# Performance work log

Hardware: AMD Instinct MI355X
Metric: run time of the kernel (lower is better)

## Reference

```python
import jax, jax.numpy as jnp
import numpy as np

N_NODES = 100000
N_EDGES = 1600000
NUM_FEATURES = 100
HIDDEN = 32
OUT = 2
DROP_P = 0.2


def setup_inputs() -> dict:
    key = jax.random.key(0)
    ks = jax.random.split(key, 6)
    x = jax.random.normal(ks[0], (N_NODES, NUM_FEATURES), dtype=jnp.float32)
    edge_index = jax.random.randint(ks[1], (2, N_EDGES), 0, N_NODES, dtype=jnp.int64)
    # Glorot-ish init for weights
    W1 = jax.random.normal(ks[2], (NUM_FEATURES, HIDDEN), dtype=jnp.float32) / jnp.sqrt(NUM_FEATURES)
    b1 = jnp.zeros((HIDDEN,), dtype=jnp.float32)
    W2 = jax.random.normal(ks[3], (HIDDEN, OUT), dtype=jnp.float32) / jnp.sqrt(HIDDEN)
    b2 = jnp.zeros((OUT,), dtype=jnp.float32)
    return {"x": x, "edge_index": edge_index, "W1": W1, "b1": b1, "W2": W2, "b2": b2}


def _gcn_norm(edge_index, num_nodes):
    # add self loops (fixed-size concat -> jit friendly)
    loops = jnp.arange(num_nodes, dtype=edge_index.dtype)
    src = jnp.concatenate([edge_index[0], loops])
    dst = jnp.concatenate([edge_index[1], loops])
    deg = jax.ops.segment_sum(jnp.ones_like(dst, dtype=jnp.float32), dst, num_segments=num_nodes)
    dinv = jnp.where(deg > 0, jax.lax.rsqrt(deg), 0.0)
    norm = dinv[src] * dinv[dst]  # [E+N]
    return src, dst, norm


def _gcn_conv(x, W, b, src, dst, norm, num_nodes):
    h = x @ W  # [N, d_out]
    msg = h[src] * norm[:, None]  # gather + scale
    out = jax.ops.segment_sum(msg, dst, num_segments=num_nodes)  # scatter-add
    return out + b


def reference(x, edge_index, W1, b1, W2, b2):
    n = x.shape[0]
    src, dst, norm = _gcn_norm(edge_index, n)
    h = jax.nn.relu(_gcn_conv(x, W1, b1, src, dst, norm, n))
    # deterministic dropout (p=0.2) with fixed key, inverted scaling as in F.dropout
    keep = jax.random.bernoulli(jax.random.key(42), 1.0 - DROP_P, h.shape)
    h = jnp.where(keep, h / (1.0 - DROP_P), 0.0)
    logits = _gcn_conv(h, W2, b2, src, dst, norm, n)
    return jax.nn.log_softmax(logits, axis=1)
```

## Files before the change

### kernel.cpp

```cpp
#include <hip/hip_runtime.h>
#include <stdint.h>
#include <math.h>

#define N_NODES   100000
#define N_EDGES   1600000
#define NFEAT     100
#define HIDDEN    32
#define OUTC      2

#define BUCK_BITS 7
#define BUCK_SZ   128
#define NBUCK     782
#define PADB      4096

#define PART_NB   256
#define PART_CHUNK ((N_EDGES + PART_NB - 1) / PART_NB)

typedef float fx4 __attribute__((ext_vector_type(4)));

__device__ __forceinline__ uint32_t rotl32(uint32_t x, int r) {
    return (x << r) | (x >> (32 - r));
}

__device__ __forceinline__ uint32_t threefry_bits(uint32_t f) {
    const uint32_t ks0 = 0u;
    const uint32_t ks1 = 42u;
    const uint32_t ks2 = 0x1BD11BDAu ^ 0u ^ 42u;
    uint32_t x0 = 0u + ks0;
    uint32_t x1 = f  + ks1;
#define TF_ROUND(r) { x0 += x1; x1 = rotl32(x1, (r)); x1 ^= x0; }
    TF_ROUND(13) TF_ROUND(15) TF_ROUND(26) TF_ROUND(6)
    x0 += ks1; x1 += ks2 + 1u;
    TF_ROUND(17) TF_ROUND(29) TF_ROUND(16) TF_ROUND(24)
    x0 += ks2; x1 += ks0 + 2u;
    TF_ROUND(13) TF_ROUND(15) TF_ROUND(26) TF_ROUND(6)
    x0 += ks0; x1 += ks1 + 3u;
    TF_ROUND(17) TF_ROUND(29) TF_ROUND(16) TF_ROUND(24)
    x0 += ks1; x1 += ks2 + 4u;
    TF_ROUND(13) TF_ROUND(15) TF_ROUND(26) TF_ROUND(6)
    x0 += ks2; x1 += ks0 + 5u;
#undef TF_ROUND
    return x0 ^ x1;
}

__device__ __forceinline__ bool dropout_keep(uint32_t f) {
    uint32_t bits = threefry_bits(f);
    float u = __uint_as_float((bits >> 9) | 0x3f800000u) - 1.0f;
    return u < 0.8f;
}

__device__ __forceinline__ uint16_t f2bf(float f) {
    uint32_t b = __float_as_uint(f);
    uint32_t lsb = (b >> 16) & 1u;
    b += 0x7fffu + lsb;
    return (uint16_t)(b >> 16);
}
__device__ __forceinline__ float bflo(uint32_t u) {
    return __uint_as_float(u << 16);
}
__device__ __forceinline__ float bfhi(uint32_t u) {
    return __uint_as_float(u & 0xffff0000u);
}

__global__ __launch_bounds__(256) void k_init(int* __restrict__ bcur) {
    int i = blockIdx.x * 256 + threadIdx.x;
    if (i < NBUCK) bcur[i] = i * PADB;
}

__global__ __launch_bounds__(1024) void k_part(const int* __restrict__ src,
                                               const int* __restrict__ dst,
                                               int* __restrict__ bcur,
                                               uint32_t* __restrict__ part) {
    __shared__ int h4[4][NBUCK];
    __shared__ int c4[4][NBUCK];
    const int t = threadIdx.x;
    const int w = (t >> 6) & 3;
    const int base = blockIdx.x * PART_CHUNK;
    const int lim = min(base + PART_CHUNK, N_EDGES);
    for (int i = t; i < 4 * NBUCK; i += 1024) ((int*)h4)[i] = 0;
    __syncthreads();
    for (int e = base + t; e < lim; e += 1024)
        atomicAdd(&h4[w][dst[e] >> BUCK_BITS], 1);
    __syncthreads();
    if (t < NBUCK) {
        int c0 = h4[0][t], c1 = h4[1][t], c2 = h4[2][t], c3 = h4[3][t];
        int tot = c0 + c1 + c2 + c3;
        int g = tot ? atomicAdd(&bcur[t], tot) : 0;
        c4[0][t] = g;
        c4[1][t] = g + c0;
        c4[2][t] = g + c0 + c1;
        c4[3][t] = g + c0 + c1 + c2;
    }
    __syncthreads();
    for (int e = base + t; e < lim; e += 1024) {
        int d = dst[e];
        int b = d >> BUCK_BITS;
        int pos = atomicAdd(&c4[w][b], 1);
        part[pos] = ((uint32_t)(d & (BUCK_SZ - 1)) << 17) | (uint32_t)src[e];
    }
}

__global__ __launch_bounds__(256) void k_sort(const uint32_t* __restrict__ part,
                                              const int* __restrict__ bcur,
                                              int* __restrict__ csr_src,
                                              int* __restrict__ rowbeg,
                                              int* __restrict__ deg,
                                              float* __restrict__ dinv) {
    __shared__ int cnt4[4][BUCK_SZ];
    __shared__ int pref[BUCK_SZ];
    __shared__ int cur4[4][BUCK_SZ];
    const int b = blockIdx.x;
    const int t = threadIdx.x;
    const int w = t >> 6;
    const int nbase = b * BUCK_SZ;
    const int bb = b * PADB;
    const int be = bcur[b];
    for (int i = t; i < 4 * BUCK_SZ; i += 256) ((int*)cnt4)[i] = 0;
    __syncthreads();
    for (int j = bb + t; j < be; j += 256)
        atomicAdd(&cnt4[w][(part[j] >> 17) & (BUCK_SZ - 1)], 1);
    __syncthreads();
    int c0 = 0, c1 = 0, c2 = 0, tot = 0;
    if (t < BUCK_SZ) {
        c0 = cnt4[0][t]; c1 = cnt4[1][t]; c2 = cnt4[2][t];
        tot = c0 + c1 + c2 + cnt4[3][t];
        pref[t] = tot;
    }
    __syncthreads();
#pragma unroll
    for (int off = 1; off < BUCK_SZ; off <<= 1) {
        int v = (t >= off && t < BUCK_SZ) ? pref[t - off] : 0;
        __syncthreads();
        if (t < BUCK_SZ) pref[t] += v;
        __syncthreads();
    }
    if (t < BUCK_SZ) {
        int ex = pref[t] - tot;
        cur4[0][t] = ex;
        cur4[1][t] = ex + c0;
        cur4[2][t] = ex + c0 + c1;
        cur4[3][t] = ex + c0 + c1 + c2;
        int node = nbase + t;
        if (node < N_NODES) {
            rowbeg[node] = bb + ex;
            deg[node] = tot;
            dinv[node] = rsqrtf((float)(tot + 1));
        }
    }
    __syncthreads();
    for (int j = bb + t; j < be; j += 256) {
        uint32_t v = part[j];
        int dl = (v >> 17) & (BUCK_SZ - 1);
        int pos = bb + atomicAdd(&cur4[w][dl], 1);
        csr_src[pos] = (int)(v & 0x1FFFF);
    }
}

__global__ __launch_bounds__(256) void k_gemm1(const float* __restrict__ x,
                                               const float* __restrict__ W1,
                                               const float* __restrict__ dinv,
                                               uint16_t* __restrict__ h0b) {
    __shared__ __align__(16) float w1s[NFEAT * HIDDEN];
    __shared__ __align__(16) float xs[32 * NFEAT];
    const int tid = threadIdx.x;
    for (int i = tid; i < NFEAT * HIDDEN / 4; i += 256)
        ((fx4*)w1s)[i] = ((const fx4*)W1)[i];
    const int row0 = blockIdx.x * 32;
    const fx4* xb = (const fx4*)(x + (size_t)row0 * NFEAT);
    for (int i = tid; i < 800; i += 256)
        ((fx4*)xs)[i] = __builtin_nontemporal_load(&xb[i]);
    __syncthreads();
    const int c = tid & 31, r0 = tid >> 5;
    float a0 = 0.f, a1 = 0.f, a2 = 0.f, a3 = 0.f;
#pragma unroll 4
    for (int k = 0; k < NFEAT; ++k) {
        float wv = w1s[k * HIDDEN + c];
        a0 = fmaf(xs[(r0)      * NFEAT + k], wv, a0);
        a1 = fmaf(xs[(r0 + 8)  * NFEAT + k], wv, a1);
        a2 = fmaf(xs[(r0 + 16) * NFEAT + k], wv, a2);
        a3 = fmaf(xs[(r0 + 24) * NFEAT + k], wv, a3);
    }
    const int r = row0 + r0;
    h0b[(size_t)(r)      * HIDDEN + c] = f2bf(a0 * dinv[r]);
    h0b[(size_t)(r + 8)  * HIDDEN + c] = f2bf(a1 * dinv[r + 8]);
    h0b[(size_t)(r + 16) * HIDDEN + c] = f2bf(a2 * dinv[r + 16]);
    h0b[(size_t)(r + 24) * HIDDEN + c] = f2bf(a3 * dinv[r + 24]);
}

__global__ __launch_bounds__(256) void k_l1(const int* __restrict__ rowbeg,
                                            const int* __restrict__ deg,
                                            const int* __restrict__ csr_src,
                                            const float* __restrict__ dinv,
                                            const uint2* __restrict__ h0u,
                                            const float* __restrict__ b1,
                                            const float* __restrict__ W2,
                                            float* __restrict__ h2s) {
    const int t = blockIdx.x * 256 + threadIdx.x;
    const int n = t >> 3;
    const int l = t & 7;
    uint2 self = h0u[(size_t)n * 8 + l];
    float aL0 = bflo(self.x), aH0 = bfhi(self.x);
    float aL1 = bflo(self.y), aH1 = bfhi(self.y);
    const int beg = rowbeg[n];
    const int d = deg[n];
    const int end = beg + d;
    const int mainEnd = beg + (d & ~3);
    int j = beg;
    int s0, s1, s2, s3;
    if (j < mainEnd) {
        s0 = csr_src[j]; s1 = csr_src[j + 1];
        s2 = csr_src[j + 2]; s3 = csr_src[j + 3];
    }
    for (; j < mainEnd; j += 4) {
        uint2 u0 = h0u[(size_t)s0 * 8 + l];
        uint2 u1 = h0u[(size_t)s1 * 8 + l];
        uint2 u2 = h0u[(size_t)s2 * 8 + l];
        uint2 u3 = h0u[(size_t)s3 * 8 + l];
        int pj = (j + 8 <= mainEnd) ? j + 4 : beg;
        s0 = csr_src[pj];     s1 = csr_src[pj + 1];
        s2 = csr_src[pj + 2]; s3 = csr_src[pj + 3];
        aL0 += bflo(u0.x); aH0 += bfhi(u0.x); aL1 += bflo(u0.y); aH1 += bfhi(u0.y);
        aL0 += bflo(u1.x); aH0 += bfhi(u1.x); aL1 += bflo(u1.y); aH1 += bfhi(u1.y);
        aL0 += bflo(u2.x); aH0 += bfhi(u2.x); aL1 += bflo(u2.y); aH1 += bfhi(u2.y);
        aL0 += bflo(u3.x); aH0 += bfhi(u3.x); aL1 += bflo(u3.y); aH1 += bfhi(u3.y);
    }
    for (; j < end; ++j) {
        uint2 u = h0u[(size_t)csr_src[j] * 8 + l];
        aL0 += bflo(u.x); aH0 += bfhi(u.x); aL1 += bflo(u.y); aH1 += bfhi(u.y);
    }
    const int c0 = 4 * l, c1 = c0 + 1, c2 = c0 + 2, c3 = c0 + 3;
    const float din = dinv[n];
    float v0 = fmaxf(fmaf(aL0, din, b1[c0]), 0.0f);
    float v1 = fmaxf(fmaf(aH0, din, b1[c1]), 0.0f);
    float v2 = fmaxf(fmaf(aL1, din, b1[c2]), 0.0f);
    float v3 = fmaxf(fmaf(aH1, din, b1[c3]), 0.0f);
    const uint32_t fb = (uint32_t)(n * HIDDEN);
    v0 = dropout_keep(fb + c0) ? v0 * 1.25f : 0.0f;
    v1 = dropout_keep(fb + c1) ? v1 * 1.25f : 0.0f;
    v2 = dropout_keep(fb + c2) ? v2 * 1.25f : 0.0f;
    v3 = dropout_keep(fb + c3) ? v3 * 1.25f : 0.0f;
    float p0 = v0 * W2[c0 * 2] + v1 * W2[c1 * 2] + v2 * W2[c2 * 2] + v3 * W2[c3 * 2];
    float p1 = v0 * W2[c0 * 2 + 1] + v1 * W2[c1 * 2 + 1] + v2 * W2[c2 * 2 + 1] + v3 * W2[c3 * 2 + 1];
#pragma unroll
    for (int m = 4; m >= 1; m >>= 1) {
        p0 += __shfl_xor(p0, m);
        p1 += __shfl_xor(p1, m);
    }
    if (l == 0) {
        float2* o = (float2*)(h2s + (size_t)n * 2);
        *o = make_float2(p0 * din, p1 * din);
    }
}

__global__ __launch_bounds__(256) void k_l2(const int* __restrict__ rowbeg,
                                            const int* __restrict__ deg,
                                            const int* __restrict__ csr_src,
                                            const float* __restrict__ dinv,
                                            const float* __restrict__ h2s,
                                            const float* __restrict__ b2,
                                            float* __restrict__ out) {
    int t = blockIdx.x * 256 + threadIdx.x;
    int n = t >> 3;
    int l = t & 7;
    if (n >= N_NODES) return;
    float acc0 = 0.0f, acc1 = 0.0f;
    float bcc0 = 0.0f, bcc1 = 0.0f;
    if (l == 0) {
        float2 hn = ((const float2*)h2s)[n];
        acc0 = hn.x; acc1 = hn.y;
    }
    const int beg = rowbeg[n];
    const int end = beg + deg[n];
    int j = beg + l;
    for (; j + 8 < end; j += 16) {
        int s0 = __builtin_nontemporal_load(&csr_src[j]);
        int s1 = __builtin_nontemporal_load(&csr_src[j + 8]);
        float2 h0v = ((const float2*)h2s)[s0];
        float2 h1v = ((const float2*)h2s)[s1];
        acc0 += h0v.x; acc1 += h0v.y;
        bcc0 += h1v.x; bcc1 += h1v.y;
    }
    if (j < end) {
        float2 hv = ((const float2*)h2s)[__builtin_nontemporal_load(&csr_src[j])];
        acc0 += hv.x; acc1 += hv.y;
    }
    acc0 += bcc0; acc1 += bcc1;
#pragma unroll
    for (int m = 4; m >= 1; m >>= 1) {
        acc0 += __shfl_xor(acc0, m);
        acc1 += __shfl_xor(acc1, m);
    }
    if (l == 0) {
        float din = dinv[n];
        float l0 = fmaf(acc0, din, b2[0]);
        float l1 = fmaf(acc1, din, b2[1]);
        float m = fmaxf(l0, l1);
        float lse = m + logf(expf(l0 - m) + expf(l1 - m));
        float2* o = (float2*)(out + (size_t)n * 2);
        *o = make_float2(l0 - lse, l1 - lse);
    }
}

static inline size_t align_up(size_t x) { return (x + 255) & ~(size_t)255; }

extern "C" void kernel_launch(void* const* d_in, const int* in_sizes, int n_in,
                              void* d_out, int out_size, void* d_ws, size_t ws_size,
                              hipStream_t stream) {
    (void)n_in; (void)in_sizes; (void)out_size; (void)ws_size;

    const float* x  = (const float*)d_in[0];
    const int*   ei = (const int*)d_in[1];
    const float* W1 = (const float*)d_in[2];
    const float* b1 = (const float*)d_in[3];
    const float* W2 = (const float*)d_in[4];
    const float* b2 = (const float*)d_in[5];
    float* out = (float*)d_out;

    const int* src = ei;
    const int* dst = ei + N_EDGES;

    char* w = (char*)d_ws;
    size_t off = 0;
    int*      bcur   = (int*)(w + off);      off += align_up((size_t)NBUCK * 4);
    int*      rowbeg = (int*)(w + off);      off += align_up((size_t)N_NODES * 4);
    int*      deg    = (int*)(w + off);      off += align_up((size_t)N_NODES * 4);
    float*    dinv   = (float*)(w + off);    off += align_up((size_t)N_NODES * 4);
    uint32_t* part   = (uint32_t*)(w + off); off += align_up((size_t)NBUCK * PADB * 4);
    int*      csr    = (int*)(w + off);      off += align_up((size_t)NBUCK * PADB * 4);
    uint16_t* h0b    = (uint16_t*)(w + off); off += align_up((size_t)N_NODES * HIDDEN * 2);
    float*    h2s    = (float*)(w + off);    off += align_up((size_t)N_NODES * OUTC * 4);

    const int B = 256;
    k_init <<<(NBUCK + B - 1) / B, B, 0, stream>>>(bcur);
    k_part <<<PART_NB, 1024, 0, stream>>>(src, dst, bcur, part);
    k_sort <<<NBUCK, B, 0, stream>>>(part, bcur, csr, rowbeg, deg, dinv);
    k_gemm1<<<N_NODES / 32, B, 0, stream>>>(x, W1, dinv, h0b);
    k_l1   <<<N_NODES / 32, B, 0, stream>>>(rowbeg, deg, csr, dinv, (const uint2*)h0b, b1, W2, h2s);
    k_l2   <<<(N_NODES * 8 + B - 1) / B, B, 0, stream>>>(rowbeg, deg, csr, dinv, h2s, b2, out);
}
```

Baseline: 178.7 us.

## Cache edges in registers for partition/sort and use 16-byte gathers in layer-1

The partition and bucket-sort kernels now load each edge once into a fixed array of register slots during the histogram pass. They reuse those values in the scatter pass instead of reading src/dst/part from global memory a second time. The layer-1 aggregation kernel now uses 4 lanes per node with uint4 (8 bf16) gathers instead of 8 lanes with uint2, with a shorter shuffle reduction. The slot counts assume each block's chunk fits in 7×1024 edges and each bucket in 4096 entries. The added registers may lower occupancy.

New measurement: 181.3 us. About the same (+1.4%).

```diff
diff --git a/kernel.cpp b/kernel.cpp
--- a/kernel.cpp
+++ b/kernel.cpp
@@ -15,6 +15,8 @@
 
 #define PART_NB   256
 #define PART_CHUNK ((N_EDGES + PART_NB - 1) / PART_NB)
+#define PART_SLOTS 7
+#define SORT_SLOTS 16
 
 typedef float fx4 __attribute__((ext_vector_type(4)));
 
@@ -79,8 +81,18 @@
     const int lim = min(base + PART_CHUNK, N_EDGES);
     for (int i = t; i < 4 * NBUCK; i += 1024) ((int*)h4)[i] = 0;
     __syncthreads();
-    for (int e = base + t; e < lim; e += 1024)
-        atomicAdd(&h4[w][dst[e] >> BUCK_BITS], 1);
+    uint32_t ed[PART_SLOTS];
+    int      eb[PART_SLOTS];
+#pragma unroll
+    for (int k = 0; k < PART_SLOTS; ++k) {
+        int e = base + t + k * 1024;
+        bool v = e < lim;
+        int d = v ? dst[e] : 0;
+        int s = v ? src[e] : 0;
+        eb[k] = v ? (d >> BUCK_BITS) : -1;
+        ed[k] = ((uint32_t)(d & (BUCK_SZ - 1)) << 17) | (uint32_t)s;
+        if (v) atomicAdd(&h4[w][d >> BUCK_BITS], 1);
+    }
     __syncthreads();
     if (t < NBUCK) {
         int c0 = h4[0][t], c1 = h4[1][t], c2 = h4[2][t], c3 = h4[3][t];
@@ -92,11 +104,12 @@
         c4[3][t] = g + c0 + c1 + c2;
     }
     __syncthreads();
-    for (int e = base + t; e < lim; e += 1024) {
-        int d = dst[e];
-        int b = d >> BUCK_BITS;
-        int pos = atomicAdd(&c4[w][b], 1);
-        part[pos] = ((uint32_t)(d & (BUCK_SZ - 1)) << 17) | (uint32_t)src[e];
+#pragma unroll
+    for (int k = 0; k < PART_SLOTS; ++k) {
+        if (eb[k] >= 0) {
+            int pos = atomicAdd(&c4[w][eb[k]], 1);
+            part[pos] = ed[k];
+        }
     }
 }
 
@@ -117,8 +130,15 @@
     const int be = bcur[b];
     for (int i = t; i < 4 * BUCK_SZ; i += 256) ((int*)cnt4)[i] = 0;
     __syncthreads();
-    for (int j = bb + t; j < be; j += 256)
-        atomicAdd(&cnt4[w][(part[j] >> 17) & (BUCK_SZ - 1)], 1);
+    uint32_t ed[SORT_SLOTS];
+#pragma unroll
+    for (int k = 0; k < SORT_SLOTS; ++k) {
+        int j = bb + t + k * 256;
+        bool v = j < be;
+        uint32_t val = v ? part[j] : 0xFFFFFFFFu;
+        ed[k] = val;
+        if (v) atomicAdd(&cnt4[w][(val >> 17) & (BUCK_SZ - 1)], 1);
+    }
     __syncthreads();
     int c0 = 0, c1 = 0, c2 = 0, tot = 0;
     if (t < BUCK_SZ) {
@@ -148,11 +168,13 @@
         }
     }
     __syncthreads();
-    for (int j = bb + t; j < be; j += 256) {
-        uint32_t v = part[j];
-        int dl = (v >> 17) & (BUCK_SZ - 1);
-        int pos = bb + atomicAdd(&cur4[w][dl], 1);
-        csr_src[pos] = (int)(v & 0x1FFFF);
+#pragma unroll
+    for (int k = 0; k < SORT_SLOTS; ++k) {
+        if (ed[k] != 0xFFFFFFFFu) {
+            int dl = (ed[k] >> 17) & (BUCK_SZ - 1);
+            int pos = bb + atomicAdd(&cur4[w][dl], 1);
+            csr_src[pos] = (int)(ed[k] & 0x1FFFF);
+        }
     }
 }
 
@@ -191,16 +213,19 @@
                                             const int* __restrict__ deg,
                                             const int* __restrict__ csr_src,
                                             const float* __restrict__ dinv,
-                                            const uint2* __restrict__ h0u,
+                                            const uint4* __restrict__ h0u,
                                             const float* __restrict__ b1,
                                             const float* __restrict__ W2,
                                             float* __restrict__ h2s) {
     const int t = blockIdx.x * 256 + threadIdx.x;
-    const int n = t >> 3;
-    const int l = t & 7;
-    uint2 self = h0u[(size_t)n * 8 + l];
+    const int n = t >> 2;
+    const int l = t & 3;
+    if (n >= N_NODES) return;
+    uint4 self = h0u[(size_t)n * 4 + l];
     float aL0 = bflo(self.x), aH0 = bfhi(self.x);
     float aL1 = bflo(self.y), aH1 = bfhi(self.y);
+    float aL2 = bflo(self.z), aH2 = bfhi(self.z);
+    float aL3 = bflo(self.w), aH3 = bfhi(self.w);
     const int beg = rowbeg[n];
     const int d = deg[n];
     const int end = beg + d;
@@ -212,37 +237,56 @@
         s2 = csr_src[j + 2]; s3 = csr_src[j + 3];
     }
     for (; j < mainEnd; j += 4) {
-        uint2 u0 = h0u[(size_t)s0 * 8 + l];
-        uint2 u1 = h0u[(size_t)s1 * 8 + l];
-        uint2 u2 = h0u[(size_t)s2 * 8 + l];
-        uint2 u3 = h0u[(size_t)s3 * 8 + l];
+        uint4 u0 = h0u[(size_t)s0 * 4 + l];
+        uint4 u1 = h0u[(size_t)s1 * 4 + l];
+        uint4 u2 = h0u[(size_t)s2 * 4 + l];
+        uint4 u3 = h0u[(size_t)s3 * 4 + l];
         int pj = (j + 8 <= mainEnd) ? j + 4 : beg;
         s0 = csr_src[pj];     s1 = csr_src[pj + 1];
         s2 = csr_src[pj + 2]; s3 = csr_src[pj + 3];
         aL0 += bflo(u0.x); aH0 += bfhi(u0.x); aL1 += bflo(u0.y); aH1 += bfhi(u0.y);
+        aL2 += bflo(u0.z); aH2 += bfhi(u0.z); aL3 += bflo(u0.w); aH3 += bfhi(u0.w);
         aL0 += bflo(u1.x); aH0 += bfhi(u1.x); aL1 += bflo(u1.y); aH1 += bfhi(u1.y);
+        aL2 += bflo(u1.z); aH2 += bfhi(u1.z); aL3 += bflo(u1.w); aH3 += bfhi(u1.w);
         aL0 += bflo(u2.x); aH0 += bfhi(u2.x); aL1 += bflo(u2.y); aH1 += bfhi(u2.y);
+        aL2 += bflo(u2.z); aH2 += bfhi(u2.z); aL3 += bflo(u2.w); aH3 += bfhi(u2.w);
         aL0 += bflo(u3.x); aH0 += bfhi(u3.x); aL1 += bflo(u3.y); aH1 += bfhi(u3.y);
+        aL2 += bflo(u3.z); aH2 += bfhi(u3.z); aL3 += bflo(u3.w); aH3 += bfhi(u3.w);
     }
     for (; j < end; ++j) {
-        uint2 u = h0u[(size_t)csr_src[j] * 8 + l];
+        uint4 u = h0u[(size_t)csr_src[j] * 4 + l];
         aL0 += bflo(u.x); aH0 += bfhi(u.x); aL1 += bflo(u.y); aH1 += bfhi(u.y);
-    }
-    const int c0 = 4 * l, c1 = c0 + 1, c2 = c0 + 2, c3 = c0 + 3;
+        aL2 += bflo(u.z); aH2 += bfhi(u.z); aL3 += bflo(u.w); aH3 += bfhi(u.w);
+    }
+    const int c0 = 8 * l;
     const float din = dinv[n];
-    float v0 = fmaxf(fmaf(aL0, din, b1[c0]), 0.0f);
-    float v1 = fmaxf(fmaf(aH0, din, b1[c1]), 0.0f);
-    float v2 = fmaxf(fmaf(aL1, din, b1[c2]), 0.0f);
-    float v3 = fmaxf(fmaf(aH1, din, b1[c3]), 0.0f);
-    const uint32_t fb = (uint32_t)(n * HIDDEN);
-    v0 = dropout_keep(fb + c0) ? v0 * 1.25f : 0.0f;
-    v1 = dropout_keep(fb + c1) ? v1 * 1.25f : 0.0f;
-    v2 = dropout_keep(fb + c2) ? v2 * 1.25f : 0.0f;
-    v3 = dropout_keep(fb + c3) ? v3 * 1.25f : 0.0f;
-    float p0 = v0 * W2[c0 * 2] + v1 * W2[c1 * 2] + v2 * W2[c2 * 2] + v3 * W2[c3 * 2];
-    float p1 = v0 * W2[c0 * 2 + 1] + v1 * W2[c1 * 2 + 1] + v2 * W2[c2 * 2 + 1] + v3 * W2[c3 * 2 + 1];
-#pragma unroll
-    for (int m = 4; m >= 1; m >>= 1) {
+    float v0 = fmaxf(fmaf(aL0, din, b1[c0 + 0]), 0.0f);
+    float v1 = fmaxf(fmaf(aH0, din, b1[c0 + 1]), 0.0f);
+    float v2 = fmaxf(fmaf(aL1, din, b1[c0 + 2]), 0.0f);
+    float v3 = fmaxf(fmaf(aH1, din, b1[c0 + 3]), 0.0f);
+    float v4 = fmaxf(fmaf(aL2, din, b1[c0 + 4]), 0.0f);
+    float v5 = fmaxf(fmaf(aH2, din, b1[c0 + 5]), 0.0f);
+    float v6 = fmaxf(fmaf(aL3, din, b1[c0 + 6]), 0.0f);
+    float v7 = fmaxf(fmaf(aH3, din, b1[c0 + 7]), 0.0f);
+    const uint32_t fb = (uint32_t)(n * HIDDEN + c0);
+    v0 = dropout_keep(fb + 0) ? v0 * 1.25f : 0.0f;
+    v1 = dropout_keep(fb + 1) ? v1 * 1.25f : 0.0f;
+    v2 = dropout_keep(fb + 2) ? v2 * 1.25f : 0.0f;
+    v3 = dropout_keep(fb + 3) ? v3 * 1.25f : 0.0f;
+    v4 = dropout_keep(fb + 4) ? v4 * 1.25f : 0.0f;
+    v5 = dropout_keep(fb + 5) ? v5 * 1.25f : 0.0f;
+    v6 = dropout_keep(fb + 6) ? v6 * 1.25f : 0.0f;
+    v7 = dropout_keep(fb + 7) ? v7 * 1.25f : 0.0f;
+    float p0 = v0 * W2[(c0 + 0) * 2] + v1 * W2[(c0 + 1) * 2]
+             + v2 * W2[(c0 + 2) * 2] + v3 * W2[(c0 + 3) * 2]
+             + v4 * W2[(c0 + 4) * 2] + v5 * W2[(c0 + 5) * 2]
+             + v6 * W2[(c0 + 6) * 2] + v7 * W2[(c0 + 7) * 2];
+    float p1 = v0 * W2[(c0 + 0) * 2 + 1] + v1 * W2[(c0 + 1) * 2 + 1]
+             + v2 * W2[(c0 + 2) * 2 + 1] + v3 * W2[(c0 + 3) * 2 + 1]
+             + v4 * W2[(c0 + 4) * 2 + 1] + v5 * W2[(c0 + 5) * 2 + 1]
+             + v6 * W2[(c0 + 6) * 2 + 1] + v7 * W2[(c0 + 7) * 2 + 1];
+#pragma unroll
+    for (int m = 2; m >= 1; m >>= 1) {
         p0 += __shfl_xor(p0, m);
         p1 += __shfl_xor(p1, m);
     }
@@ -335,6 +379,6 @@
     k_part <<<PART_NB, 1024, 0, stream>>>(src, dst, bcur, part);
     k_sort <<<NBUCK, B, 0, stream>>>(part, bcur, csr, rowbeg, deg, dinv);
     k_gemm1<<<N_NODES / 32, B, 0, stream>>>(x, W1, dinv, h0b);
-    k_l1   <<<N_NODES / 32, B, 0, stream>>>(rowbeg, deg, csr, dinv, (const uint2*)h0b, b1, W2, h2s);
+    k_l1   <<<(N_NODES * 4 + B - 1) / B, B, 0, stream>>>(rowbeg, deg, csr, dinv, (const uint4*)h0b, b1, W2, h2s);
     k_l2   <<<(N_NODES * 8 + B - 1) / B, B, 0, stream>>>(rowbeg, deg, csr, dinv, h2s, b2, out);
 }
```
